# Optimization experiments

Measured on AMD Instinct MI355X. Metric: run time of the kernel, lower is better.

The kernel has to match this reference:

```python
import jax, jax.numpy as jnp
import numpy as np

DELTA = 0.1
LRELU_SLOPE = 0.01
BN_EPS = 1e-5


def ternarize(t, d):
    # {-1, 0, +1}: 0 where |t| < d, sign(t) otherwise (matches the torch where-chain)
    return jnp.where(jnp.abs(t) < d, 0.0, jnp.sign(t))


def ste_ternarize(t, d):
    # straight-through estimator, matching the torch .data-swap trick
    return t + jax.lax.stop_gradient(ternarize(t, d) - t)


def conv2d(x, w, stride, pad):
    return jax.lax.conv_general_dilated(
        x, w, (stride, stride), [(pad, pad), (pad, pad)],
        dimension_numbers=('NCHW', 'OIHW', 'NCHW'))


def batchnorm(x, gamma, beta, mean, var):
    inv = gamma / jnp.sqrt(var + BN_EPS)
    return x * inv[None, :, None, None] + (beta - mean * inv)[None, :, None, None]


def lrelu(x):
    return jnp.where(x > 0, x, LRELU_SLOPE * x)


def setup_inputs() -> dict:
    key = jax.random.key(0)
    ks = jax.random.split(key, 12)
    B, Cin, C, H, W = 16, 32, 64, 256, 256
    return {
        'x':      jax.random.normal(ks[0], (B, Cin, H, W), jnp.float32),
        'w11':    jax.random.normal(ks[1], (C, Cin, 3, 3), jnp.float32),
        'b11':    jax.random.normal(ks[2], (C,), jnp.float32),
        'w1':     jax.random.normal(ks[3], (C, Cin, 3, 3), jnp.float32),
        'b1':     jax.random.normal(ks[4], (C,), jnp.float32),
        'w2':     jax.random.normal(ks[5], (C, C, 3, 3), jnp.float32),
        'b2':     jax.random.normal(ks[6], (C,), jnp.float32),
        'gamma_p': jax.random.uniform(ks[7], (Cin,), jnp.float32),
        'beta_p':  jax.random.normal(ks[8], (Cin,), jnp.float32),
        'mean_p':  jax.random.normal(ks[9], (Cin,), jnp.float32),
        'var_p':   jnp.ones((Cin,), jnp.float32),
        'gamma1':  jax.random.uniform(ks[10], (C,), jnp.float32),
        'beta1':   jax.random.normal(ks[11], (C,), jnp.float32),
        'mean1':   jax.random.normal(jax.random.fold_in(key, 99), (C,), jnp.float32),
        'var1':    jnp.ones((C,), jnp.float32),
    }


def reference(x, w11, b11, w1, b1, w2, b2,
              gamma_p, beta_p, mean_p, var_p,
              gamma1, beta1, mean1, var1):
    # shortcut conv11 (stride 3); NOTE: torch mutates input.data in-place, so
    # the main branch below consumes the x already ternarized with d11.
    d11 = DELTA * jnp.max(jnp.abs(w11))
    x_t = ste_ternarize(x, d11)
    prev_mp = conv2d(x_t, ste_ternarize(w11, d11), 3, 1) \
        + ste_ternarize(b11, d11)[None, :, None, None]

    # main branch: pre_bn -> lrelu -> conv1 (stride 1) -> bn1 -> lrelu -> dropout(eval) -> conv2 (stride 3)
    out = lrelu(batchnorm(x_t, gamma_p, beta_p, mean_p, var_p))

    d1 = DELTA * jnp.max(jnp.abs(w1))
    out = conv2d(ste_ternarize(out, d1), ste_ternarize(w1, d1), 1, 1) \
        + ste_ternarize(b1, d1)[None, :, None, None]
    out = lrelu(batchnorm(out, gamma1, beta1, mean1, var1))
    # dropout: identity in eval mode

    d2 = DELTA * jnp.max(jnp.abs(w2))
    out = conv2d(ste_ternarize(out, d2), ste_ternarize(w2, d2), 3, 1) \
        + ste_ternarize(b2, d2)[None, :, None, None]

    return lrelu(out + prev_mp)  # [16, 64, 86, 86]
```

## Files before the change

kernel.cpp:

```cpp
#include <hip/hip_runtime.h>
#include <stdint.h>

#define B 16
#define CIN 32
#define C 64
#define H 256
#define W 256
#define OH 86
#define OW 86
#define PIX (OH*OW)

typedef int v4i __attribute__((ext_vector_type(4)));

#define OFF_D      0
#define OFF_MAPW   64
#define OFF_S1     256
#define OFF_SH1    512
#define OFF_B11    768
#define OFF_B1     1024
#define OFF_B2     1280
#define OFF_W11R   4096
#define OFF_W1R    24576
#define OFF_W2R    45056
#define OFF_XTP    262144
#define OFF_XMAP   33816576

__device__ __forceinline__ int tern_i(float t, float d) {
    return (fabsf(t) < d) ? 0 : (t > 0.f ? 1 : -1);
}

__global__ void k_zero(unsigned* d) {
    if (threadIdx.x < 3) d[threadIdx.x] = 0u;
}

__global__ __launch_bounds__(256) void k_absmax(const float* w11, const float* w1,
                                                const float* w2, unsigned* dws) {
    __shared__ unsigned red[256];
    int b = blockIdx.x >> 4, sub = blockIdx.x & 15;
    const float* p = (b == 0) ? w11 : (b == 1) ? w1 : w2;
    int n = (b == 2) ? 36864 : 18432;
    int chunk = (n + 15) >> 4;
    int lo = sub * chunk, hi = min(lo + chunk, n);
    unsigned m = 0;
    for (int i = lo + threadIdx.x; i < hi; i += 256)
        m = max(m, __float_as_uint(fabsf(p[i])));
    red[threadIdx.x] = m; __syncthreads();
    for (int s = 128; s > 0; s >>= 1) {
        if (threadIdx.x < s) red[threadIdx.x] = max(red[threadIdx.x], red[threadIdx.x + s]);
        __syncthreads();
    }
    if (threadIdx.x == 0) atomicMax(&dws[b], red[0]);
}

__global__ __launch_bounds__(256) void k_prep(const float* w11, const float* w1, const float* w2,
                                              const float* b11, const float* b1, const float* b2,
                                              const float* gp, const float* bp, const float* mp, const float* vp,
                                              const float* g1, const float* be1, const float* me1, const float* v1,
                                              char* ws) {
    const unsigned* dw = (const unsigned*)(ws + OFF_D);
    float d11 = __fmul_rn(0.1f, __uint_as_float(dw[0]));
    float d1  = __fmul_rn(0.1f, __uint_as_float(dw[1]));
    float d2v = __fmul_rn(0.1f, __uint_as_float(dw[2]));
    int idx = blockIdx.x * 256 + threadIdx.x;
    if (idx < 4608) {
        int j = idx & 3, c16 = (idx >> 2) & 15, cot = (idx >> 6) & 1;
        int h = (idx >> 7) & 1, q1 = (idx >> 8) & 1, pos = idx >> 9;
        int co = h * 32 + cot * 16 + c16;
        unsigned wd = 0;
        #pragma unroll
        for (int jj = 0; jj < 4; jj++) {
            int ci = q1 * 16 + j * 4 + jj;
            int tv = tern_i(w1[(co * 32 + ci) * 9 + pos], d1);
            wd |= ((unsigned)(tv & 255)) << (8 * jj);
        }
        ((int*)(ws + OFF_W1R))[idx] = (int)wd;
    } else if (idx < 9216) {
        int i2 = idx - 4608;
        int j = i2 & 3, c16 = (i2 >> 2) & 15, cot = (i2 >> 6) & 3;
        int q1 = (i2 >> 8) & 1, pos = i2 >> 9;
        int co = cot * 16 + c16;
        unsigned wd = 0;
        #pragma unroll
        for (int jj = 0; jj < 4; jj++) {
            int ci = q1 * 16 + j * 4 + jj;
            int tv = tern_i(w11[(co * 32 + ci) * 9 + pos], d11);
            wd |= ((unsigned)(tv & 255)) << (8 * jj);
        }
        ((int*)(ws + OFF_W11R))[i2] = (int)wd;
    } else if (idx < 18432) {
        int i2 = idx - 9216;
        int j = i2 & 3, c16 = (i2 >> 2) & 15, cot = (i2 >> 6) & 3;
        int q1 = (i2 >> 8) & 1, h = (i2 >> 9) & 1, pos = i2 >> 10;
        int co = cot * 16 + c16;
        unsigned wd = 0;
        #pragma unroll
        for (int jj = 0; jj < 4; jj++) {
            int ci = h * 32 + q1 * 16 + j * 4 + jj;
            int tv = tern_i(w2[(co * 64 + ci) * 9 + pos], d2v);
            wd |= ((unsigned)(tv & 255)) << (8 * jj);
        }
        ((int*)(ws + OFF_W2R))[i2] = (int)wd;
    } else {
        int i = idx - 18432;
        if (i < 64) {
            ((int*)(ws + OFF_B11))[i] = tern_i(b11[i], d11);
        } else if (i < 128) {
            ((int*)(ws + OFF_B1))[i - 64] = tern_i(b1[i - 64], d1);
        } else if (i < 192) {
            ((int*)(ws + OFF_B2))[i - 128] = tern_i(b2[i - 128], d2v);
        } else if (i < 216) {
            int j = i - 192;
            int g = j / 3, s = j % 3;
            float v = (float)(s - 1);
            unsigned wd = 0;
            #pragma unroll
            for (int jj = 0; jj < 4; jj++) {
                int c = g * 4 + jj;
                float inv = __fdiv_rn(gp[c], __fsqrt_rn(__fadd_rn(vp[c], 1e-5f)));
                float sh  = __fsub_rn(bp[c], __fmul_rn(mp[c], inv));
                float z   = __fadd_rn(__fmul_rn(v, inv), sh);
                z = (z > 0.f) ? z : __fmul_rn(0.01f, z);
                wd |= ((unsigned)(tern_i(z, d1) & 255)) << (8 * jj);
            }
            ((int*)(ws + OFF_MAPW))[j] = (int)wd;
        } else if (i < 280) {
            int c = i - 216;
            float inv = __fdiv_rn(g1[c], __fsqrt_rn(__fadd_rn(v1[c], 1e-5f)));
            ((float*)(ws + OFF_S1))[c]  = inv;
            ((float*)(ws + OFF_SH1))[c] = __fsub_rn(be1[c], __fmul_rn(me1[c], inv));
        }
    }
}

__global__ __launch_bounds__(256) void k_tern_x(const float* __restrict__ x,
                                                char* __restrict__ ws) {
    float d11 = __fmul_rn(0.1f, __uint_as_float(((const unsigned*)(ws + OFF_D))[0]));
    const int* mapw = (const int*)(ws + OFF_MAPW);
    int idx = blockIdx.x * 256 + threadIdx.x;
    int pix = idx & 65535, n = idx >> 16;
    int gx = pix & 255;
    const float* xp = x + ((size_t)n * CIN << 16) + pix;
    int rw[8], mw[8];
    #pragma unroll
    for (int g = 0; g < 8; ++g) {
        unsigned r = 0, m = 0;
        #pragma unroll
        for (int j = 0; j < 4; ++j) {
            float v = xp[(size_t)(g * 4 + j) << 16];
            int tv = tern_i(v, d11);
            r |= ((unsigned)(tv & 255)) << (8 * j);
            m |= (((unsigned)mapw[g * 3 + tv + 1] >> (8 * j)) & 255u) << (8 * j);
        }
        rw[g] = (int)r; mw[g] = (int)m;
    }
    int4* o1 = (int4*)(ws + OFF_XTP) + ((size_t)idx * 2);
    o1[0] = make_int4(rw[0], rw[1], rw[2], rw[3]);
    o1[1] = make_int4(rw[4], rw[5], rw[6], rw[7]);
    int f = (gx & 1) ^ ((gx >> 2) & 1);
    int4* o2 = (int4*)(ws + OFF_XMAP) + ((size_t)idx * 2);
    o2[f]     = make_int4(mw[0], mw[1], mw[2], mw[3]);
    o2[f ^ 1] = make_int4(mw[4], mw[5], mw[6], mw[7]);
}

#define T2S 12
__global__ __launch_bounds__(256) void k_net(const char* __restrict__ ws,
                                             float* __restrict__ out) {
    __shared__ int mapL[676 * 8];
    __shared__ int t2L[576 * T2S];
    int tid = threadIdx.x, bid = blockIdx.x;
    int tx = bid % 11; int tt = bid / 11; int ty = tt % 11; int n = tt / 11;
    int OH0 = ty * 8, OW0 = tx * 8;
    int Y0 = OH0 * 3 - 2, X0 = OW0 * 3 - 2;
    int c16 = tid & 15, q = (tid >> 4) & 3, wv = tid >> 6;
    int q1 = q & 1, qh = q >> 1;
    const int* xmapn = (const int*)(ws + OFF_XMAP + ((size_t)n << 21));
    const int* xtpn  = (const int*)(ws + OFF_XTP  + ((size_t)n << 21));

    for (int i = tid; i < 1352; i += 256) {
        int pix = i >> 1, hf = i & 1;
        int my = pix / 26, mx = pix - my * 26;
        int gy = Y0 + my, gxv = X0 + mx;
        int4 v = make_int4(0, 0, 0, 0);
        if ((unsigned)gy < H && (unsigned)gxv < W)
            v = *(const int4*)&xmapn[(gy * 256 + gxv) * 8 + hf * 4];
        *(int4*)&mapL[pix * 8 + hf * 4] = v;
    }

    int o = wv * 16 + c16;
    int oh8 = o >> 3, ow8 = o & 7;
    int gOH = OH0 + oh8, gOW = OW0 + ow8;
    bool pvalid = (gOH < OH) && (gOW < OW);
    const int* w11r = (const int*)(ws + OFF_W11R);
    v4i acc11[4];
    {
        v4i a[5];
        #pragma unroll
        for (int c = 0; c < 5; ++c) {
            int pos = 2 * c + qh;
            v4i z = {0, 0, 0, 0};
            if (pos < 9) {
                int kh = pos / 3, kw = pos - kh * 3;
                int ih = gOH * 3 - 1 + kh, iw = gOW * 3 - 1 + kw;
                if (pvalid && (unsigned)ih < H && (unsigned)iw < W)
                    z = *(const v4i*)&xtpn[(ih * 256 + iw) * 8 + q1 * 4];
            }
            a[c] = z;
        }
        #pragma unroll
        for (int cot = 0; cot < 4; ++cot) {
            v4i acc = {0, 0, 0, 0};
            #pragma unroll
            for (int c = 0; c < 5; ++c) {
                int pos = 2 * c + qh;
                v4i b = {0, 0, 0, 0};
                if (pos < 9)
                    b = *(const v4i*)&w11r[((pos * 2 + q1) * 4 + cot) * 64 + c16 * 4];
                acc = __builtin_amdgcn_mfma_i32_16x16x64_i8(a[c], b, acc, 0, 0, 0);
            }
            acc11[cot] = acc;
        }
    }
    __syncthreads();

    const int* w1r = (const int*)(ws + OFF_W1R);
    const int* w2r = (const int*)(ws + OFF_W2R);
    const int* b1i = (const int*)(ws + OFF_B1);
    const float* s1 = (const float*)(ws + OFF_S1);
    const float* sh1 = (const float*)(ws + OFF_SH1);
    float d2v = __fmul_rn(0.1f, __uint_as_float(((const unsigned*)(ws + OFF_D))[2]));
    v4i acc2[4];
    #pragma unroll
    for (int cot = 0; cot < 4; ++cot) { v4i z = {0,0,0,0}; acc2[cot] = z; }

    #pragma unroll 1
    for (int h = 0; h < 2; ++h) {
        v4i bw1[5][2];
        int b1c[2]; float s1c[2], sh1c[2];
        #pragma unroll
        for (int cot = 0; cot < 2; ++cot) {
            int co = h * 32 + cot * 16 + c16;
            b1c[cot] = b1i[co]; s1c[cot] = s1[co]; sh1c[cot] = sh1[co];
        }
        #pragma unroll
        for (int c = 0; c < 5; ++c) {
            int pos = 2 * c + qh;
            #pragma unroll
            for (int cot = 0; cot < 2; ++cot) {
                v4i z = {0, 0, 0, 0};
                if (pos < 9)
                    z = *(const v4i*)&w1r[(((pos * 2 + q1) * 2 + h) * 2 + cot) * 64 + c16 * 4];
                bw1[c][cot] = z;
            }
        }
        #pragma unroll 1
        for (int pg = 0; pg < 9; ++pg) {
            int pbase = (wv * 9 + pg) * 16;
            int fp = pbase + c16;
            int iy = fp / 24, ix = fp - iy * 24;
            v4i a[5];
            #pragma unroll
            for (int c = 0; c < 5; ++c) {
                int pos = 2 * c + qh;
                v4i z = {0, 0, 0, 0};
                if (pos < 9) {
                    int kh = pos / 3, kw = pos - kh * 3;
                    int my = iy + kh, mx = ix + kw;
                    int gxl = X0 + mx;
                    int hb = q1 ^ ((gxl & 1) ^ ((gxl >> 2) & 1));
                    z = *(const v4i*)&mapL[(my * 26 + mx) * 8 + hb * 4];
                }
                a[c] = z;
            }
            int pwr = pbase + q * 4 + (c16 & 3);
            int wy = pwr / 24, wx = pwr - wy * 24;
            bool wok = ((unsigned)(Y0 + 1 + wy) < H) && ((unsigned)(X0 + 1 + wx) < W);
            #pragma unroll
            for (int cot = 0; cot < 2; ++cot) {
                v4i acc = {0, 0, 0, 0};
                #pragma unroll
                for (int c = 0; c < 5; ++c)
                    acc = __builtin_amdgcn_mfma_i32_16x16x64_i8(a[c], bw1[c][cot], acc, 0, 0, 0);
                unsigned wcol = 0;
                #pragma unroll
                for (int i = 0; i < 4; ++i) {
                    int vi = acc[i] + b1c[cot];
                    float z = __fadd_rn(__fmul_rn((float)vi, s1c[cot]), sh1c[cot]);
                    z = (z > 0.f) ? z : __fmul_rn(0.01f, z);
                    int tv = (fabsf(z) < d2v) ? 0 : (z > 0.f ? 1 : -1);
                    wcol |= ((unsigned)(tv & 255)) << (8 * i);
                }
                unsigned y1 = (unsigned)__shfl_xor((int)wcol, 1);
                unsigned z1 = ((c16 & 1) == 0)
                            ? __builtin_amdgcn_perm(y1, wcol, 0x06020400u)
                            : __builtin_amdgcn_perm(y1, wcol, 0x03070105u);
                unsigned y2 = (unsigned)__shfl_xor((int)z1, 2);
                unsigned r  = ((c16 & 2) == 0)
                            ? __builtin_amdgcn_perm(y2, z1, 0x05040100u)
                            : __builtin_amdgcn_perm(y2, z1, 0x03020706u);
                t2L[pwr * T2S + cot * 4 + (c16 >> 2)] = wok ? (int)r : 0;
            }
        }
        __syncthreads();
        {
            v4i a2[5];
            #pragma unroll
            for (int c = 0; c < 5; ++c) {
                int pos = 2 * c + qh;
                v4i z = {0, 0, 0, 0};
                if (pos < 9) {
                    int kh = pos / 3, kw = pos - kh * 3;
                    int p2 = (oh8 * 3 + kh) * 24 + (ow8 * 3 + kw);
                    z = *(const v4i*)&t2L[p2 * T2S + q1 * 4];
                }
                a2[c] = z;
            }
            #pragma unroll
            for (int cot = 0; cot < 4; ++cot) {
                v4i acc = acc2[cot];
                #pragma unroll
                for (int c = 0; c < 5; ++c) {
                    int pos = 2 * c + qh;
                    v4i b = {0, 0, 0, 0};
                    if (pos < 9)
                        b = *(const v4i*)&w2r[((((pos * 2 + h) * 2 + q1) * 4 + cot)) * 64 + c16 * 4];
                    acc = __builtin_amdgcn_mfma_i32_16x16x64_i8(a2[c], b, acc, 0, 0, 0);
                }
                acc2[cot] = acc;
            }
        }
        __syncthreads();
    }

    const int* b2i = (const int*)(ws + OFF_B2);
    const int* b11i = (const int*)(ws + OFF_B11);
    int pt0 = wv * 16 + q * 4;
    int ohh = OH0 + (pt0 >> 3);
    int oww = OW0 + (pt0 & 7);
    if (ohh < OH) {
        #pragma unroll
        for (int cot = 0; cot < 4; ++cot) {
            int co = cot * 16 + c16;
            int bc = b2i[co] + b11i[co];
            float f[4];
            #pragma unroll
            for (int i = 0; i < 4; ++i) {
                float z = (float)(acc2[cot][i] + acc11[cot][i] + bc);
                f[i] = (z > 0.f) ? z : __fmul_rn(0.01f, z);
            }
            float* op = out + ((size_t)(n * 64 + co)) * PIX + ohh * OW + oww;
            if (oww + 3 < OW) {
                *(float4*)op = make_float4(f[0], f[1], f[2], f[3]);
            } else {
                #pragma unroll
                for (int i = 0; i < 4; ++i)
                    if (oww + i < OW) op[i] = f[i];
            }
        }
    }
}

extern "C" void kernel_launch(void* const* d_in, const int* in_sizes, int n_in,
                              void* d_out, int out_size, void* d_ws, size_t ws_size,
                              hipStream_t stream) {
    const float* x    = (const float*)d_in[0];
    const float* w11  = (const float*)d_in[1];
    const float* b11  = (const float*)d_in[2];
    const float* w1   = (const float*)d_in[3];
    const float* b1   = (const float*)d_in[4];
    const float* w2   = (const float*)d_in[5];
    const float* b2   = (const float*)d_in[6];
    const float* gp   = (const float*)d_in[7];
    const float* bp   = (const float*)d_in[8];
    const float* mp   = (const float*)d_in[9];
    const float* vp   = (const float*)d_in[10];
    const float* g1   = (const float*)d_in[11];
    const float* be1  = (const float*)d_in[12];
    const float* me1  = (const float*)d_in[13];
    const float* v1   = (const float*)d_in[14];
    char* ws = (char*)d_ws;
    float* out = (float*)d_out;

    k_zero<<<1, 64, 0, stream>>>((unsigned*)(ws + OFF_D));
    k_absmax<<<48, 256, 0, stream>>>(w11, w1, w2, (unsigned*)(ws + OFF_D));
    k_prep<<<74, 256, 0, stream>>>(w11, w1, w2, b11, b1, b2,
                                   gp, bp, mp, vp, g1, be1, me1, v1, ws);
    k_tern_x<<<4096, 256, 0, stream>>>(x, ws);
    k_net<<<11 * 11 * B, 256, 0, stream>>>(ws, out);
}
```

Baseline: 149.7 us.

## Precompute integer thresholds for BN+ternarize and restructure conv pipeline with padded inputs

Replaces the per-element float batchnorm, leaky-ReLU and ternarize step after conv1 with two integer thresholds per channel, found in the prep kernel by scanning the possible accumulator values. Inputs are written into a zero-padded 272x272 layout so the main kernel reads them straight from global memory without bounds checks, and the shared-memory staging of the mapped input is dropped. conv1 now produces all 64 channels in one pass, and conv2 runs afterwards in a single 9-tap sweep over the full 64 input channels, replacing the two-half loop. This adds a padding kernel and larger workspace buffers and sets occupancy launch bounds, but it relies on the accumulator range staying within the scanned threshold window.

```diff
diff --git a/kernel.cpp b/kernel.cpp
--- a/kernel.cpp
+++ b/kernel.cpp
@@ -9,28 +9,44 @@
 #define OH 86
 #define OW 86
 #define PIX (OH*OW)
+#define PADW 272
+#define PWORDS (PADW*PADW*8)
 
 typedef int v4i __attribute__((ext_vector_type(4)));
 
 #define OFF_D      0
 #define OFF_MAPW   64
-#define OFF_S1     256
-#define OFF_SH1    512
 #define OFF_B11    768
-#define OFF_B1     1024
 #define OFF_B2     1280
+#define OFF_TLO    1536
+#define OFF_THI    1792
 #define OFF_W11R   4096
 #define OFF_W1R    24576
 #define OFF_W2R    45056
 #define OFF_XTP    262144
-#define OFF_XMAP   33816576
+#define OFF_XMAP   38141952
 
 __device__ __forceinline__ int tern_i(float t, float d) {
     return (fabsf(t) < d) ? 0 : (t > 0.f ? 1 : -1);
 }
 
-__global__ void k_zero(unsigned* d) {
-    if (threadIdx.x < 3) d[threadIdx.x] = 0u;
+__global__ __launch_bounds__(256) void k_pad(char* ws) {
+    int idx = blockIdx.x * 256 + threadIdx.x;
+    if (blockIdx.x == 0 && threadIdx.x < 3)
+        ((unsigned*)(ws + OFF_D))[threadIdx.x] = 0u;
+    if (idx >= 135168) return;
+    int n = idx / 8448, c = idx - n * 8448;
+    int row, col;
+    if (c < 4352) {
+        int r = c / 272; col = c - r * 272; row = (r < 2) ? r : r + 256;
+    } else {
+        int c2 = c - 4352; int k = c2 & 15;
+        row = 2 + (c2 >> 4); col = (k < 2) ? k : k + 256;
+    }
+    size_t base = ((size_t)n * (PADW * PADW) + (size_t)row * PADW + col) * 2;
+    int4 z = make_int4(0, 0, 0, 0);
+    ((int4*)(ws + OFF_XTP))[base] = z;  ((int4*)(ws + OFF_XTP))[base + 1] = z;
+    ((int4*)(ws + OFF_XMAP))[base] = z; ((int4*)(ws + OFF_XMAP))[base + 1] = z;
 }
 
 __global__ __launch_bounds__(256) void k_absmax(const float* w11, const float* w1,
@@ -63,9 +79,9 @@
     float d2v = __fmul_rn(0.1f, __uint_as_float(dw[2]));
     int idx = blockIdx.x * 256 + threadIdx.x;
     if (idx < 4608) {
-        int j = idx & 3, c16 = (idx >> 2) & 15, cot = (idx >> 6) & 1;
-        int h = (idx >> 7) & 1, q1 = (idx >> 8) & 1, pos = idx >> 9;
-        int co = h * 32 + cot * 16 + c16;
+        int j = idx & 3, c16 = (idx >> 2) & 15, cot = (idx >> 6) & 3;
+        int q1 = (idx >> 8) & 1, pos = idx >> 9;
+        int co = cot * 16 + c16;
         unsigned wd = 0;
         #pragma unroll
         for (int jj = 0; jj < 4; jj++) {
@@ -89,13 +105,13 @@
         ((int*)(ws + OFF_W11R))[i2] = (int)wd;
     } else if (idx < 18432) {
         int i2 = idx - 9216;
-        int j = i2 & 3, c16 = (i2 >> 2) & 15, cot = (i2 >> 6) & 3;
-        int q1 = (i2 >> 8) & 1, h = (i2 >> 9) & 1, pos = i2 >> 10;
+        int j = i2 & 3, q = (i2 >> 2) & 3, c16 = (i2 >> 4) & 15;
+        int cot = (i2 >> 8) & 3, pos = i2 >> 10;
         int co = cot * 16 + c16;
         unsigned wd = 0;
         #pragma unroll
         for (int jj = 0; jj < 4; jj++) {
-            int ci = h * 32 + q1 * 16 + j * 4 + jj;
+            int ci = q * 16 + j * 4 + jj;
             int tv = tern_i(w2[(co * 64 + ci) * 9 + pos], d2v);
             wd |= ((unsigned)(tv & 255)) << (8 * jj);
         }
@@ -105,11 +121,9 @@
         if (i < 64) {
             ((int*)(ws + OFF_B11))[i] = tern_i(b11[i], d11);
         } else if (i < 128) {
-            ((int*)(ws + OFF_B1))[i - 64] = tern_i(b1[i - 64], d1);
-        } else if (i < 192) {
-            ((int*)(ws + OFF_B2))[i - 128] = tern_i(b2[i - 128], d2v);
-        } else if (i < 216) {
-            int j = i - 192;
+            ((int*)(ws + OFF_B2))[i - 64] = tern_i(b2[i - 64], d2v);
+        } else if (i < 152) {
+            int j = i - 128;
             int g = j / 3, s = j % 3;
             float v = (float)(s - 1);
             unsigned wd = 0;
@@ -123,11 +137,21 @@
                 wd |= ((unsigned)(tern_i(z, d1) & 255)) << (8 * jj);
             }
             ((int*)(ws + OFF_MAPW))[j] = (int)wd;
-        } else if (i < 280) {
-            int c = i - 216;
-            float inv = __fdiv_rn(g1[c], __fsqrt_rn(__fadd_rn(v1[c], 1e-5f)));
-            ((float*)(ws + OFF_S1))[c]  = inv;
-            ((float*)(ws + OFF_SH1))[c] = __fsub_rn(be1[c], __fmul_rn(me1[c], inv));
+        } else if (i < 216) {
+            int co = i - 152;
+            float inv = __fdiv_rn(g1[co], __fsqrt_rn(__fadd_rn(v1[co], 1e-5f)));
+            float sh  = __fsub_rn(be1[co], __fmul_rn(me1[co], inv));
+            int lo = 1000, hi = 1000;
+            for (int vi = -290; vi <= 290; ++vi) {
+                float z = __fadd_rn(__fmul_rn((float)vi, inv), sh);
+                z = (z > 0.f) ? z : __fmul_rn(0.01f, z);
+                int cls = (fabsf(z) < d2v) ? 0 : (z > 0.f ? 1 : -1);
+                if (cls >= 0 && lo == 1000) lo = vi;
+                if (cls == 1 && hi == 1000) hi = vi;
+            }
+            int b1t = tern_i(b1[co], d1);
+            ((int*)(ws + OFF_TLO))[co] = lo - b1t;
+            ((int*)(ws + OFF_THI))[co] = hi - b1t;
         }
     }
 }
@@ -138,7 +162,7 @@
     const int* mapw = (const int*)(ws + OFF_MAPW);
     int idx = blockIdx.x * 256 + threadIdx.x;
     int pix = idx & 65535, n = idx >> 16;
-    int gx = pix & 255;
+    int y = pix >> 8, xq = pix & 255;
     const float* xp = x + ((size_t)n * CIN << 16) + pix;
     int rw[8], mw[8];
     #pragma unroll
@@ -153,46 +177,51 @@
         }
         rw[g] = (int)r; mw[g] = (int)m;
     }
-    int4* o1 = (int4*)(ws + OFF_XTP) + ((size_t)idx * 2);
+    size_t base = ((size_t)n * (PADW * PADW) + (size_t)(y + 2) * PADW + (xq + 2)) * 2;
+    int4* o1 = (int4*)(ws + OFF_XTP) + base;
     o1[0] = make_int4(rw[0], rw[1], rw[2], rw[3]);
     o1[1] = make_int4(rw[4], rw[5], rw[6], rw[7]);
-    int f = (gx & 1) ^ ((gx >> 2) & 1);
-    int4* o2 = (int4*)(ws + OFF_XMAP) + ((size_t)idx * 2);
-    o2[f]     = make_int4(mw[0], mw[1], mw[2], mw[3]);
-    o2[f ^ 1] = make_int4(mw[4], mw[5], mw[6], mw[7]);
-}
-
-#define T2S 12
-__global__ __launch_bounds__(256) void k_net(const char* __restrict__ ws,
-                                             float* __restrict__ out) {
-    __shared__ int mapL[676 * 8];
-    __shared__ int t2L[576 * T2S];
+    int4* o2 = (int4*)(ws + OFF_XMAP) + base;
+    o2[0] = make_int4(mw[0], mw[1], mw[2], mw[3]);
+    o2[1] = make_int4(mw[4], mw[5], mw[6], mw[7]);
+}
+
+__global__ __launch_bounds__(256, 3) void k_net(const char* __restrict__ ws,
+                                                float* __restrict__ out) {
+    __shared__ int t2L[576 * 20];
     int tid = threadIdx.x, bid = blockIdx.x;
     int tx = bid % 11; int tt = bid / 11; int ty = tt % 11; int n = tt / 11;
     int OH0 = ty * 8, OW0 = tx * 8;
     int Y0 = OH0 * 3 - 2, X0 = OW0 * 3 - 2;
     int c16 = tid & 15, q = (tid >> 4) & 3, wv = tid >> 6;
     int q1 = q & 1, qh = q >> 1;
-    const int* xmapn = (const int*)(ws + OFF_XMAP + ((size_t)n << 21));
-    const int* xtpn  = (const int*)(ws + OFF_XTP  + ((size_t)n << 21));
-
-    for (int i = tid; i < 1352; i += 256) {
-        int pix = i >> 1, hf = i & 1;
-        int my = pix / 26, mx = pix - my * 26;
-        int gy = Y0 + my, gxv = X0 + mx;
-        int4 v = make_int4(0, 0, 0, 0);
-        if ((unsigned)gy < H && (unsigned)gxv < W)
-            v = *(const int4*)&xmapn[(gy * 256 + gxv) * 8 + hf * 4];
-        *(int4*)&mapL[pix * 8 + hf * 4] = v;
-    }
-
-    int o = wv * 16 + c16;
-    int oh8 = o >> 3, ow8 = o & 7;
-    int gOH = OH0 + oh8, gOW = OW0 + ow8;
-    bool pvalid = (gOH < OH) && (gOW < OW);
-    const int* w11r = (const int*)(ws + OFF_W11R);
-    v4i acc11[4];
-    {
+    const int* xmapn = (const int*)(ws + OFF_XMAP) + (size_t)n * PWORDS;
+    const int* xtpn  = (const int*)(ws + OFF_XTP)  + (size_t)n * PWORDS;
+
+    const int* w1r = (const int*)(ws + OFF_W1R);
+    v4i bw1[5][4];
+    #pragma unroll
+    for (int c = 0; c < 5; ++c) {
+        int pos = 2 * c + qh;
+        #pragma unroll
+        for (int ct = 0; ct < 4; ++ct) {
+            v4i z = {0, 0, 0, 0};
+            if (pos < 9) z = *(const v4i*)&w1r[((pos * 2 + q1) * 4 + ct) * 64 + c16 * 4];
+            bw1[c][ct] = z;
+        }
+    }
+    const int* TLO = (const int*)(ws + OFF_TLO);
+    const int* THI = (const int*)(ws + OFF_THI);
+    int tlo[4], thi[4];
+    #pragma unroll
+    for (int ct = 0; ct < 4; ++ct) { tlo[ct] = TLO[ct * 16 + c16]; thi[ct] = THI[ct * 16 + c16]; }
+
+    int Yb = Y0 + 2, Xb = X0 + 2;
+    #pragma unroll 1
+    for (int pg = 0; pg < 9; ++pg) {
+        int pbase = (wv * 9 + pg) * 16;
+        int fp = pbase + c16;
+        int iy = fp / 24, ix = fp - iy * 24;
         v4i a[5];
         #pragma unroll
         for (int c = 0; c < 5; ++c) {
@@ -200,135 +229,81 @@
             v4i z = {0, 0, 0, 0};
             if (pos < 9) {
                 int kh = pos / 3, kw = pos - kh * 3;
-                int ih = gOH * 3 - 1 + kh, iw = gOW * 3 - 1 + kw;
-                if (pvalid && (unsigned)ih < H && (unsigned)iw < W)
-                    z = *(const v4i*)&xtpn[(ih * 256 + iw) * 8 + q1 * 4];
+                z = *(const v4i*)&xmapn[((Yb + iy + kh) * PADW + (Xb + ix + kw)) * 8 + q1 * 4];
             }
             a[c] = z;
         }
-        #pragma unroll
-        for (int cot = 0; cot < 4; ++cot) {
+        int pwr = pbase + q * 4 + (c16 & 3);
+        int wy = pwr / 24, wx = pwr - wy * 24;
+        bool wok = ((unsigned)(Y0 + 1 + wy) < H) && ((unsigned)(X0 + 1 + wx) < W);
+        #pragma unroll
+        for (int ct = 0; ct < 4; ++ct) {
             v4i acc = {0, 0, 0, 0};
             #pragma unroll
-            for (int c = 0; c < 5; ++c) {
-                int pos = 2 * c + qh;
-                v4i b = {0, 0, 0, 0};
-                if (pos < 9)
-                    b = *(const v4i*)&w11r[((pos * 2 + q1) * 4 + cot) * 64 + c16 * 4];
-                acc = __builtin_amdgcn_mfma_i32_16x16x64_i8(a[c], b, acc, 0, 0, 0);
-            }
-            acc11[cot] = acc;
+            for (int c = 0; c < 5; ++c)
+                acc = __builtin_amdgcn_mfma_i32_16x16x64_i8(a[c], bw1[c][ct], acc, 0, 0, 0);
+            unsigned wcol = 0;
+            #pragma unroll
+            for (int i = 0; i < 4; ++i) {
+                int cls = (acc[i] >= tlo[ct] ? 1 : 0) + (acc[i] >= thi[ct] ? 1 : 0) - 1;
+                wcol |= ((unsigned)(cls & 255)) << (8 * i);
+            }
+            unsigned y1 = (unsigned)__shfl_xor((int)wcol, 1);
+            unsigned z1 = ((c16 & 1) == 0)
+                        ? __builtin_amdgcn_perm(y1, wcol, 0x06020400u)
+                        : __builtin_amdgcn_perm(y1, wcol, 0x03070105u);
+            unsigned y2 = (unsigned)__shfl_xor((int)z1, 2);
+            unsigned r  = ((c16 & 2) == 0)
+                        ? __builtin_amdgcn_perm(y2, z1, 0x05040100u)
+                        : __builtin_amdgcn_perm(y2, z1, 0x03020706u);
+            t2L[pwr * 20 + ct * 4 + (c16 >> 2)] = wok ? (int)r : 0;
         }
     }
     __syncthreads();
 
-    const int* w1r = (const int*)(ws + OFF_W1R);
+    int o = wv * 16 + c16;
+    int oh8 = o >> 3, ow8 = o & 7;
+    int gOH = OH0 + oh8, gOW = OW0 + ow8;
+    v4i a11[5];
+    #pragma unroll
+    for (int c = 0; c < 5; ++c) {
+        int pos = 2 * c + qh;
+        v4i z = {0, 0, 0, 0};
+        if (pos < 9) {
+            int kh = pos / 3, kw = pos - kh * 3;
+            int ih = gOH * 3 - 1 + kh, iw = gOW * 3 - 1 + kw;
+            z = *(const v4i*)&xtpn[((ih + 2) * PADW + (iw + 2)) * 8 + q1 * 4];
+        }
+        a11[c] = z;
+    }
+    v4i a2[9];
+    #pragma unroll
+    for (int pos = 0; pos < 9; ++pos) {
+        int kh = pos / 3, kw = pos - kh * 3;
+        int p2 = (oh8 * 3 + kh) * 24 + ow8 * 3 + kw;
+        a2[pos] = *(const v4i*)&t2L[p2 * 20 + q * 4];
+    }
     const int* w2r = (const int*)(ws + OFF_W2R);
-    const int* b1i = (const int*)(ws + OFF_B1);
-    const float* s1 = (const float*)(ws + OFF_S1);
-    const float* sh1 = (const float*)(ws + OFF_SH1);
-    float d2v = __fmul_rn(0.1f, __uint_as_float(((const unsigned*)(ws + OFF_D))[2]));
-    v4i acc2[4];
-    #pragma unroll
-    for (int cot = 0; cot < 4; ++cot) { v4i z = {0,0,0,0}; acc2[cot] = z; }
-
-    #pragma unroll 1
-    for (int h = 0; h < 2; ++h) {
-        v4i bw1[5][2];
-        int b1c[2]; float s1c[2], sh1c[2];
-        #pragma unroll
-        for (int cot = 0; cot < 2; ++cot) {
-            int co = h * 32 + cot * 16 + c16;
-            b1c[cot] = b1i[co]; s1c[cot] = s1[co]; sh1c[cot] = sh1[co];
-        }
+    const int* w11r = (const int*)(ws + OFF_W11R);
+    v4i acc2[4], acc11[4];
+    #pragma unroll
+    for (int ct = 0; ct < 4; ++ct) {
+        v4i acc = {0, 0, 0, 0};
+        #pragma unroll
+        for (int pos = 0; pos < 9; ++pos) {
+            v4i b = *(const v4i*)&w2r[((pos * 4 + ct) * 16 + c16) * 16 + q * 4];
+            acc = __builtin_amdgcn_mfma_i32_16x16x64_i8(a2[pos], b, acc, 0, 0, 0);
+        }
+        acc2[ct] = acc;
+        v4i acc1 = {0, 0, 0, 0};
         #pragma unroll
         for (int c = 0; c < 5; ++c) {
             int pos = 2 * c + qh;
-            #pragma unroll
-            for (int cot = 0; cot < 2; ++cot) {
-                v4i z = {0, 0, 0, 0};
-                if (pos < 9)
-                    z = *(const v4i*)&w1r[(((pos * 2 + q1) * 2 + h) * 2 + cot) * 64 + c16 * 4];
-                bw1[c][cot] = z;
-            }
-        }
-        #pragma unroll 1
-        for (int pg = 0; pg < 9; ++pg) {
-            int pbase = (wv * 9 + pg) * 16;
-            int fp = pbase + c16;
-            int iy = fp / 24, ix = fp - iy * 24;
-            v4i a[5];
-            #pragma unroll
-            for (int c = 0; c < 5; ++c) {
-                int pos = 2 * c + qh;
-                v4i z = {0, 0, 0, 0};
-                if (pos < 9) {
-                    int kh = pos / 3, kw = pos - kh * 3;
-                    int my = iy + kh, mx = ix + kw;
-                    int gxl = X0 + mx;
-                    int hb = q1 ^ ((gxl & 1) ^ ((gxl >> 2) & 1));
-                    z = *(const v4i*)&mapL[(my * 26 + mx) * 8 + hb * 4];
-                }
-                a[c] = z;
-            }
-            int pwr = pbase + q * 4 + (c16 & 3);
-            int wy = pwr / 24, wx = pwr - wy * 24;
-            bool wok = ((unsigned)(Y0 + 1 + wy) < H) && ((unsigned)(X0 + 1 + wx) < W);
-            #pragma unroll
-            for (int cot = 0; cot < 2; ++cot) {
-                v4i acc = {0, 0, 0, 0};
-                #pragma unroll
-                for (int c = 0; c < 5; ++c)
-                    acc = __builtin_amdgcn_mfma_i32_16x16x64_i8(a[c], bw1[c][cot], acc, 0, 0, 0);
-                unsigned wcol = 0;
-                #pragma unroll
-                for (int i = 0; i < 4; ++i) {
-                    int vi = acc[i] + b1c[cot];
-                    float z = __fadd_rn(__fmul_rn((float)vi, s1c[cot]), sh1c[cot]);
-                    z = (z > 0.f) ? z : __fmul_rn(0.01f, z);
-                    int tv = (fabsf(z) < d2v) ? 0 : (z > 0.f ? 1 : -1);
-                    wcol |= ((unsigned)(tv & 255)) << (8 * i);
-                }
-                unsigned y1 = (unsigned)__shfl_xor((int)wcol, 1);
-                unsigned z1 = ((c16 & 1) == 0)
-                            ? __builtin_amdgcn_perm(y1, wcol, 0x06020400u)
-                            : __builtin_amdgcn_perm(y1, wcol, 0x03070105u);
-                unsigned y2 = (unsigned)__shfl_xor((int)z1, 2);
-                unsigned r  = ((c16 & 2) == 0)
-                            ? __builtin_amdgcn_perm(y2, z1, 0x05040100u)
-                            : __builtin_amdgcn_perm(y2, z1, 0x03020706u);
-                t2L[pwr * T2S + cot * 4 + (c16 >> 2)] = wok ? (int)r : 0;
-            }
-        }
-        __syncthreads();
-        {
-            v4i a2[5];
-            #pragma unroll
-            for (int c = 0; c < 5; ++c) {
-                int pos = 2 * c + qh;
-                v4i z = {0, 0, 0, 0};
-                if (pos < 9) {
-                    int kh = pos / 3, kw = pos - kh * 3;
-                    int p2 = (oh8 * 3 + kh) * 24 + (ow8 * 3 + kw);
-                    z = *(const v4i*)&t2L[p2 * T2S + q1 * 4];
-                }
-                a2[c] = z;
-            }
-            #pragma unroll
-            for (int cot = 0; cot < 4; ++cot) {
-                v4i acc = acc2[cot];
-                #pragma unroll
-                for (int c = 0; c < 5; ++c) {
-                    int pos = 2 * c + qh;
-                    v4i b = {0, 0, 0, 0};
-                    if (pos < 9)
-                        b = *(const v4i*)&w2r[((((pos * 2 + h) * 2 + q1) * 4 + cot)) * 64 + c16 * 4];
-                    acc = __builtin_amdgcn_mfma_i32_16x16x64_i8(a2[c], b, acc, 0, 0, 0);
-                }
-                acc2[cot] = acc;
-            }
-        }
-        __syncthreads();
+            v4i b = {0, 0, 0, 0};
+            if (pos < 9) b = *(const v4i*)&w11r[((pos * 2 + q1) * 4 + ct) * 64 + c16 * 4];
+            acc1 = __builtin_amdgcn_mfma_i32_16x16x64_i8(a11[c], b, acc1, 0, 0, 0);
+        }
+        acc11[ct] = acc1;
     }
 
     const int* b2i = (const int*)(ws + OFF_B2);
@@ -338,13 +313,13 @@
     int oww = OW0 + (pt0 & 7);
     if (ohh < OH) {
         #pragma unroll
-        for (int cot = 0; cot < 4; ++cot) {
-            int co = cot * 16 + c16;
+        for (int ct = 0; ct < 4; ++ct) {
+            int co = ct * 16 + c16;
             int bc = b2i[co] + b11i[co];
             float f[4];
             #pragma unroll
             for (int i = 0; i < 4; ++i) {
-                float z = (float)(acc2[cot][i] + acc11[cot][i] + bc);
+                float z = (float)(acc2[ct][i] + acc11[ct][i] + bc);
                 f[i] = (z > 0.f) ? z : __fmul_rn(0.01f, z);
             }
             float* op = out + ((size_t)(n * 64 + co)) * PIX + ohh * OW + oww;
@@ -380,9 +355,9 @@
     char* ws = (char*)d_ws;
     float* out = (float*)d_out;
 
-    k_zero<<<1, 64, 0, stream>>>((unsigned*)(ws + OFF_D));
+    k_pad<<<528, 256, 0, stream>>>(ws);
     k_absmax<<<48, 256, 0, stream>>>(w11, w1, w2, (unsigned*)(ws + OFF_D));
-    k_prep<<<74, 256, 0, stream>>>(w11, w1, w2, b11, b1, b2,
+    k_prep<<<73, 256, 0, stream>>>(w11, w1, w2, b11, b1, b2,
                                    gp, bp, mp, vp, g1, be1, me1, v1, ws);
     k_tern_x<<<4096, 256, 0, stream>>>(x, ws);
     k_net<<<11 * 11 * B, 256, 0, stream>>>(ws, out);
```

Result: faster. 144.0 us (-3.8%).
